# Kernel tuning notes

Hardware: AMD Instinct MI355X
Metric: run time of the kernel (lower is better)

## Reference

```python
import jax, jax.numpy as jnp
import numpy as np

D_MODEL = 128
NUM_LAYERS = 2
D_FF = 512
VOCAB = 128
OUT_DIM = 10
B, S = 512, 256
EPS_FEAT = 1e-6
LN_EPS = 1e-5


def _pos_encoding(seq_len, d):
    pos = jnp.arange(seq_len, dtype=jnp.float32)[:, None]            # [S,1]
    div = jnp.exp(jnp.arange(0, d, 2, dtype=jnp.float32) * (-np.log(10000.0) / d))
    ang = pos * div                                                   # [S,D/2]
    pe = jnp.stack([jnp.sin(ang), jnp.cos(ang)], axis=-1).reshape(seq_len, d)
    return pe[:, None, :]                                             # [S,1,D]


def _layer_norm(x, g, b):
    mu = jnp.mean(x, axis=-1, keepdims=True)
    var = jnp.mean(jnp.square(x - mu), axis=-1, keepdims=True)
    return (x - mu) * jax.lax.rsqrt(var + LN_EPS) * g + b


def setup_inputs() -> dict:
    key = jax.random.key(0)
    ks = jax.random.split(key, 20)
    sc = 0.02
    inp = {
        'src': jax.random.randint(ks[0], (B, S), 0, VOCAB),
        'emb': jax.random.normal(ks[1], (VOCAB, D_MODEL), jnp.float32) * sc,
        'wq': jax.random.normal(ks[2], (NUM_LAYERS, D_MODEL, D_MODEL), jnp.float32) * sc,
        'bq': jnp.zeros((NUM_LAYERS, D_MODEL), jnp.float32),
        'wk': jax.random.normal(ks[3], (NUM_LAYERS, D_MODEL, D_MODEL), jnp.float32) * sc,
        'bk': jnp.zeros((NUM_LAYERS, D_MODEL), jnp.float32),
        'wv': jax.random.normal(ks[4], (NUM_LAYERS, D_MODEL, D_MODEL), jnp.float32) * sc,
        'bv': jnp.zeros((NUM_LAYERS, D_MODEL), jnp.float32),
        'w1': jax.random.normal(ks[5], (NUM_LAYERS, D_FF, D_MODEL), jnp.float32) * sc,
        'b1': jnp.zeros((NUM_LAYERS, D_FF), jnp.float32),
        'w2': jax.random.normal(ks[6], (NUM_LAYERS, D_MODEL, D_FF), jnp.float32) * sc,
        'b2': jnp.zeros((NUM_LAYERS, D_MODEL), jnp.float32),
        'g1': jnp.ones((NUM_LAYERS, D_MODEL), jnp.float32),
        'beta1': jnp.zeros((NUM_LAYERS, D_MODEL), jnp.float32),
        'g2': jnp.ones((NUM_LAYERS, D_MODEL), jnp.float32),
        'beta2': jnp.zeros((NUM_LAYERS, D_MODEL), jnp.float32),
        'fc_w': jax.random.normal(ks[7], (OUT_DIM, D_MODEL), jnp.float32) * sc,
        'fc_b': jnp.zeros((OUT_DIM,), jnp.float32),
    }
    return inp


def reference(src, emb, wq, bq, wk, bk, wv, bv, w1, b1, w2, b2,
              g1, beta1, g2, beta2, fc_w, fc_b):
    # src: [B,S] int -> permute -> [S,B]
    x = emb[src.T] * np.sqrt(float(D_MODEL))          # [S,B,D]
    x = x + _pos_encoding(x.shape[0], D_MODEL)
    for l in range(NUM_LAYERS):
        # Linear attention (faithful to original: einsum 'b' axis = seq here)
        Q = jax.nn.relu(jnp.einsum('sbd,ed->sbe', x, wq[l]) + bq[l]) + EPS_FEAT
        K = jax.nn.relu(jnp.einsum('sbd,ed->sbe', x, wk[l]) + bk[l]) + EPS_FEAT
        V = jnp.einsum('sbd,ed->sbe', x, wv[l]) + bv[l]
        KV = jnp.einsum('snd,sne->sde', K, V)         # [S,D,D] (n = batch axis)
        Z = 1.0 / (jnp.einsum('snd,sd->sn', Q, K.sum(axis=1)) + EPS_FEAT)  # [S,B]
        attn = jnp.einsum('snd,sde,sn->sne', Q, KV, Z)  # [S,B,D]
        x = _layer_norm(x + attn, g1[l], beta1[l])
        ff = jnp.einsum('sbf,df->sbd',
                        jax.nn.relu(jnp.einsum('sbd,fd->sbf', x, w1[l]) + b1[l]),
                        w2[l]) + b2[l]
        x = _layer_norm(x + ff, g2[l], beta2[l])
    x = jnp.transpose(x, (1, 0, 2))                   # [B,S,D]
    pooled = jnp.mean(x, axis=1)                      # [B,D]
    return pooled @ fc_w.T + fc_b                     # [B,OUT]
```

## Files before the change

### kernel.cpp

```cpp
#include <hip/hip_runtime.h>

typedef unsigned short u16;
typedef unsigned int u32;
typedef short bf16x8 __attribute__((ext_vector_type(8)));
typedef float f32x4 __attribute__((ext_vector_type(4)));

__device__ __forceinline__ float b2f(u16 v) { return __uint_as_float(((u32)v) << 16); }
__device__ __forceinline__ u16 f2b(float f) {
    u32 x = __float_as_uint(f);
    return (u16)((x + 0x7fffu + ((x >> 16) & 1u)) >> 16);
}
__device__ __forceinline__ float lo16(u32 w) { return __uint_as_float(w << 16); }
__device__ __forceinline__ float hi16(u32 w) { return __uint_as_float(w & 0xffff0000u); }

#define S_LEN 256
#define B_SZ  512
#define DM    128
#define DFF   512
#define MROWS (S_LEN * B_SZ)

__device__ __forceinline__ int sw16(int r, int d) {
    return r * 128 + ((((d >> 3) ^ (r & 15)) & 15) << 3) + (d & 7);
}

__global__ __launch_bounds__(256) void detect_kernel(const u32* __restrict__ embw,
                                                     int* __restrict__ flag) {
    int z = 0, big = 0;
    for (int i = threadIdx.x; i < 8192; i += 256) {
        u32 w = embw[i];
        u32 lo = w & 0xffffu;
        if (lo == 0u) z++;
        else if (((lo >> 7) & 0xffu) >= 0xC0u) big++;
    }
#pragma unroll
    for (int off = 32; off > 0; off >>= 1) {
        z   += __shfl_xor(z, off, 64);
        big += __shfl_xor(big, off, 64);
    }
    __shared__ int zz[4], bb[4];
    if ((threadIdx.x & 63) == 0) { zz[threadIdx.x >> 6] = z; bb[threadIdx.x >> 6] = big; }
    __syncthreads();
    if (threadIdx.x == 0) {
        int Z = zz[0] + zz[1] + zz[2] + zz[3];
        int Bc = bb[0] + bb[1] + bb[2] + bb[3];
        flag[0] = (Z > 4096 || Bc > 16) ? 1 : 0;
    }
}

struct Ptrs { const void* p[17]; };

__global__ __launch_bounds__(256) void convert_kernel(Ptrs ps, u16* __restrict__ canon,
                                                      const int* __restrict__ flag) {
    const int cnt[17] = {16384,32768,256,32768,256,32768,256,131072,1024,131072,
                         256,256,256,256,256,1280,10};
    const int off[17] = {0,16384,49152,49408,82176,82432,115200,115456,246528,
                         247552,378624,378880,379136,379392,379648,379904,381184};
    const int bst[18] = {0,8,24,25,41,42,58,59,123,124,188,189,190,191,192,193,194,195};
    const int isf = *flag;
    const int blk = blockIdx.x;
    int idx = 0;
#pragma unroll
    for (int i = 0; i < 17; ++i) if (blk >= bst[i + 1]) idx = i + 1;
    const int local = blk - bst[idx];
    const int n = cnt[idx];
    const void* sp = ps.p[idx];
    u16* dp = canon + off[idx];
#pragma unroll
    for (int j = 0; j < 8; ++j) {
        int e = local * 2048 + j * 256 + threadIdx.x;
        if (e < n) {
            u16 v = isf ? f2b(((const float*)sp)[e]) : ((const u16*)sp)[e];
            dp[e] = v;
        }
    }
}

__global__ __launch_bounds__(256) void embed_kernel(const int* __restrict__ src,
                                                    const u16* __restrict__ emb,
                                                    u16* __restrict__ X) {
    int idx = blockIdx.x * 256 + threadIdx.x;
    int d2 = idx & 63;
    int m = idx >> 6;
    int s = m >> 9;
    int b = m & 511;
    int tok = src[b * S_LEN + s];
    int d = d2 * 2;
    float e0 = b2f(emb[tok * DM + d])     * 11.3137084989847604f;
    float e1 = b2f(emb[tok * DM + d + 1]) * 11.3137084989847604f;
    float ang = (float)s * expf((float)d * -0.0719557841560639f);
    float v0 = e0 + sinf(ang);
    float v1 = e1 + cosf(ang);
    u32 w = (u32)f2b(v0) | ((u32)f2b(v1) << 16);
    *(u32*)(X + (size_t)m * DM + d) = w;
}

__global__ __launch_bounds__(256) void kvproj_kernel(
    const u16* __restrict__ X, const u16* __restrict__ Wk, const u16* __restrict__ bk,
    const u16* __restrict__ Wv, const u16* __restrict__ bv,
    u16* __restrict__ KVt, float* __restrict__ Ksum)
{
    __shared__ __align__(16) char sm_[49152];
    u16* Xs = (u16*)sm_;
    u16* Kt = (u16*)(sm_ + 16384);
    u16* Vt = (u16*)(sm_ + 32768);
    const int s = blockIdx.x, t = threadIdx.x;
    const int w = t >> 6, quad = (t >> 4) & 3, lr = t & 15;
    const u16* Xg = X + (size_t)s * B_SZ * DM;

    bf16x8 wkf[2][4], wvf[2][4];
    float kb[2], vb[2];
#pragma unroll
    for (int ct = 0; ct < 2; ++ct) {
        int e = w * 32 + ct * 16 + lr;
#pragma unroll
        for (int kc = 0; kc < 4; ++kc) {
            wkf[ct][kc] = *(const bf16x8*)(Wk + e * 128 + kc * 32 + quad * 8);
            wvf[ct][kc] = *(const bf16x8*)(Wv + e * 128 + kc * 32 + quad * 8);
        }
        kb[ct] = b2f(bk[e]);
        vb[ct] = b2f(bv[e]);
    }

    const f32x4 z4 = {0.f, 0.f, 0.f, 0.f};
    f32x4 kvacc[2][8];
#pragma unroll
    for (int dt = 0; dt < 2; ++dt)
#pragma unroll
        for (int ct = 0; ct < 8; ++ct) kvacc[dt][ct] = z4;
    float ks[2] = {0.f, 0.f};

    for (int b0 = 0; b0 < B_SZ; b0 += 64) {
        __syncthreads();
#pragma unroll
        for (int i = 0; i < 4; ++i) {
            int e8 = (i * 256 + t) * 8; int r = e8 >> 7, k0 = e8 & 127;
            *(uint4*)(Xs + sw16(r, k0)) = *(const uint4*)(Xg + (size_t)(b0 + r) * DM + k0);
        }
        __syncthreads();
        f32x4 pa[4][2];
#pragma unroll
        for (int mt = 0; mt < 4; ++mt) { pa[mt][0] = z4; pa[mt][1] = z4; }
#pragma unroll
        for (int kc = 0; kc < 4; ++kc) {
            bf16x8 a[4];
#pragma unroll
            for (int mt = 0; mt < 4; ++mt)
                a[mt] = *(const bf16x8*)(Xs + sw16(mt * 16 + lr, kc * 32 + quad * 8));
#pragma unroll
            for (int ct = 0; ct < 2; ++ct)
#pragma unroll
                for (int mt = 0; mt < 4; ++mt)
                    pa[mt][ct] = __builtin_amdgcn_mfma_f32_16x16x32_bf16(a[mt], wkf[ct][kc], pa[mt][ct], 0, 0, 0);
        }
#pragma unroll
        for (int ct = 0; ct < 2; ++ct) {
            int e = w * 32 + ct * 16 + lr, e7 = e & 7;
#pragma unroll
            for (int mt = 0; mt < 4; ++mt) {
                u16 h[4]; float ssum = 0.f;
#pragma unroll
                for (int j = 0; j < 4; ++j) {
                    float v = fmaxf(pa[mt][ct][j] + kb[ct], 0.f) + 1e-6f;
                    h[j] = f2b(v); ssum += b2f(h[j]);
                }
                ks[ct] += ssum;
                uint2 pk; pk.x = (u32)h[0] | ((u32)h[1] << 16); pk.y = (u32)h[2] | ((u32)h[3] << 16);
                int bs = mt * 2 + (quad >> 1);
                *(uint2*)(Kt + e * 64 + (((bs ^ e7) & 7) << 3) + (quad & 1) * 4) = pk;
            }
        }
#pragma unroll
        for (int mt = 0; mt < 4; ++mt) { pa[mt][0] = z4; pa[mt][1] = z4; }
#pragma unroll
        for (int kc = 0; kc < 4; ++kc) {
            bf16x8 a[4];
#pragma unroll
            for (int mt = 0; mt < 4; ++mt)
                a[mt] = *(const bf16x8*)(Xs + sw16(mt * 16 + lr, kc * 32 + quad * 8));
#pragma unroll
            for (int ct = 0; ct < 2; ++ct)
#pragma unroll
                for (int mt = 0; mt < 4; ++mt)
                    pa[mt][ct] = __builtin_amdgcn_mfma_f32_16x16x32_bf16(a[mt], wvf[ct][kc], pa[mt][ct], 0, 0, 0);
        }
#pragma unroll
        for (int ct = 0; ct < 2; ++ct) {
            int e = w * 32 + ct * 16 + lr, e7 = e & 7;
#pragma unroll
            for (int mt = 0; mt < 4; ++mt) {
                u16 h[4];
#pragma unroll
                for (int j = 0; j < 4; ++j) h[j] = f2b(pa[mt][ct][j] + vb[ct]);
                uint2 pk; pk.x = (u32)h[0] | ((u32)h[1] << 16); pk.y = (u32)h[2] | ((u32)h[3] << 16);
                int bs = mt * 2 + (quad >> 1);
                *(uint2*)(Vt + e * 64 + (((bs ^ e7) & 7) << 3) + (quad & 1) * 4) = pk;
            }
        }
        __syncthreads();
#pragma unroll
        for (int kc = 0; kc < 2; ++kc) {
            bf16x8 ka[2];
#pragma unroll
            for (int dt = 0; dt < 2; ++dt) {
                int d = (2 * w + dt) * 16 + lr;
                ka[dt] = *(const bf16x8*)(Kt + d * 64 + ((((kc * 4 + quad) ^ (d & 7)) & 7) << 3));
            }
#pragma unroll
            for (int ct = 0; ct < 8; ++ct) {
                int e = ct * 16 + lr;
                bf16x8 vf = *(const bf16x8*)(Vt + e * 64 + ((((kc * 4 + quad) ^ (e & 7)) & 7) << 3));
                kvacc[0][ct] = __builtin_amdgcn_mfma_f32_16x16x32_bf16(ka[0], vf, kvacc[0][ct], 0, 0, 0);
                kvacc[1][ct] = __builtin_amdgcn_mfma_f32_16x16x32_bf16(ka[1], vf, kvacc[1][ct], 0, 0, 0);
            }
        }
    }
#pragma unroll
    for (int ct = 0; ct < 2; ++ct) {
        float v = ks[ct];
        v += __shfl_xor(v, 16, 64);
        v += __shfl_xor(v, 32, 64);
        if (quad == 0) Ksum[s * 128 + w * 32 + ct * 16 + lr] = v;
    }
    u16* KVg = KVt + (size_t)s * (DM * DM);
#pragma unroll
    for (int dt = 0; dt < 2; ++dt) {
        int d0 = (2 * w + dt) * 16 + quad * 4;
#pragma unroll
        for (int ct = 0; ct < 8; ++ct) {
            int e = ct * 16 + lr;
            u16 h[4];
#pragma unroll
            for (int j = 0; j < 4; ++j) h[j] = f2b(kvacc[dt][ct][j]);
            uint2 pk; pk.x = (u32)h[0] | ((u32)h[1] << 16); pk.y = (u32)h[2] | ((u32)h[3] << 16);
            *(uint2*)(KVg + e * 128 + d0) = pk;
        }
    }
}

__global__ __launch_bounds__(256) void attn_ln_kernel(
    const u16* X, const u16* __restrict__ Wq, const u16* __restrict__ bq,
    const u16* __restrict__ KVt, const float* __restrict__ Ksum,
    u16* Xout, const u16* __restrict__ g, const u16* __restrict__ beta)
{
    __shared__ __align__(16) char sm_[65536];
    u16* R1 = (u16*)sm_;
    u16* R2 = (u16*)(sm_ + 32768);
    const int blk = blockIdx.x, s = blk >> 2, rc = blk & 3, t = threadIdx.x;
    const int w = t >> 6, quad = (t >> 4) & 3, lr = t & 15;
    const size_t m0 = (size_t)s * B_SZ + rc * 128;

#pragma unroll
    for (int i = 0; i < 8; ++i) {
        int e8 = (i * 256 + t) * 8; int r = e8 >> 7, k0 = e8 & 127;
        *(uint4*)(R1 + sw16(r, k0)) = *(const uint4*)(Wq + e8);
        *(uint4*)(R2 + sw16(r, k0)) = *(const uint4*)(X + (m0 + r) * DM + k0);
    }
    __syncthreads();
    const f32x4 z4 = {0.f, 0.f, 0.f, 0.f};
    f32x4 qacc[2][8];
#pragma unroll
    for (int mt = 0; mt < 2; ++mt)
#pragma unroll
        for (int ct = 0; ct < 8; ++ct) qacc[mt][ct] = z4;
#pragma unroll
    for (int kc = 0; kc < 4; ++kc) {
        bf16x8 a[2];
#pragma unroll
        for (int mt = 0; mt < 2; ++mt)
            a[mt] = *(const bf16x8*)(R2 + sw16(w * 32 + mt * 16 + lr, kc * 32 + quad * 8));
#pragma unroll
        for (int ct = 0; ct < 8; ++ct) {
            bf16x8 wf = *(const bf16x8*)(R1 + sw16(ct * 16 + lr, kc * 32 + quad * 8));
            qacc[0][ct] = __builtin_amdgcn_mfma_f32_16x16x32_bf16(a[0], wf, qacc[0][ct], 0, 0, 0);
            qacc[1][ct] = __builtin_amdgcn_mfma_f32_16x16x32_bf16(a[1], wf, qacc[1][ct], 0, 0, 0);
        }
    }
    __syncthreads();
    float ksm[8], bqv[8];
#pragma unroll
    for (int ct = 0; ct < 8; ++ct) {
        ksm[ct] = Ksum[s * 128 + ct * 16 + lr];
        bqv[ct] = b2f(bq[ct * 16 + lr]);
    }
    float zden[2][4];
#pragma unroll
    for (int mt = 0; mt < 2; ++mt)
#pragma unroll
        for (int j = 0; j < 4; ++j) zden[mt][j] = 0.f;
#pragma unroll
    for (int mt = 0; mt < 2; ++mt)
#pragma unroll
        for (int ct = 0; ct < 8; ++ct) {
            int d = ct * 16 + lr;
#pragma unroll
            for (int j = 0; j < 4; ++j) {
                float qv = fmaxf(qacc[mt][ct][j] + bqv[ct], 0.f) + 1e-6f;
                u16 qb16 = f2b(qv);
                zden[mt][j] += b2f(qb16) * ksm[ct];
                int b = w * 32 + mt * 16 + quad * 4 + j;
                R1[sw16(b, d)] = qb16;
            }
        }
#pragma unroll
    for (int mt = 0; mt < 2; ++mt)
#pragma unroll
        for (int j = 0; j < 4; ++j) {
            float v = zden[mt][j];
            v += __shfl_xor(v, 1, 64); v += __shfl_xor(v, 2, 64);
            v += __shfl_xor(v, 4, 64); v += __shfl_xor(v, 8, 64);
            zden[mt][j] = 1.f / (v + 1e-6f);
        }
    const u16* KVg = KVt + (size_t)s * (DM * DM);
#pragma unroll
    for (int i = 0; i < 8; ++i) {
        int e8 = (i * 256 + t) * 8; int r = e8 >> 7, k0 = e8 & 127;
        *(uint4*)(R2 + sw16(r, k0)) = *(const uint4*)(KVg + e8);
    }
    __syncthreads();
    f32x4 oacc[2][8];
#pragma unroll
    for (int mt = 0; mt < 2; ++mt)
#pragma unroll
        for (int ct = 0; ct < 8; ++ct) oacc[mt][ct] = z4;
#pragma unroll
    for (int kc = 0; kc < 4; ++kc) {
        bf16x8 qa[2];
#pragma unroll
        for (int mt = 0; mt < 2; ++mt)
            qa[mt] = *(const bf16x8*)(R1 + sw16(w * 32 + mt * 16 + lr, kc * 32 + quad * 8));
#pragma unroll
        for (int ct = 0; ct < 8; ++ct) {
            bf16x8 kf = *(const bf16x8*)(R2 + sw16(ct * 16 + lr, kc * 32 + quad * 8));
            oacc[0][ct] = __builtin_amdgcn_mfma_f32_16x16x32_bf16(qa[0], kf, oacc[0][ct], 0, 0, 0);
            oacc[1][ct] = __builtin_amdgcn_mfma_f32_16x16x32_bf16(qa[1], kf, oacc[1][ct], 0, 0, 0);
        }
    }
    float gv[8], bev[8];
#pragma unroll
    for (int ct = 0; ct < 8; ++ct) {
        gv[ct]  = b2f(g[ct * 16 + lr]);
        bev[ct] = b2f(beta[ct * 16 + lr]);
    }
#pragma unroll
    for (int mt = 0; mt < 2; ++mt)
#pragma unroll
        for (int j = 0; j < 4; ++j) {
            int b = w * 32 + mt * 16 + quad * 4 + j;
            const u16* xr = X + (m0 + b) * DM;
            float vals[8], sum = 0.f, sq = 0.f;
#pragma unroll
            for (int ct = 0; ct < 8; ++ct) {
                float v = fmaf(oacc[mt][ct][j], zden[mt][j], b2f(xr[ct * 16 + lr]));
                vals[ct] = v; sum += v; sq += v * v;
            }
            sum += __shfl_xor(sum, 1, 64); sq += __shfl_xor(sq, 1, 64);
            sum += __shfl_xor(sum, 2, 64); sq += __shfl_xor(sq, 2, 64);
            sum += __shfl_xor(sum, 4, 64); sq += __shfl_xor(sq, 4, 64);
            sum += __shfl_xor(sum, 8, 64); sq += __shfl_xor(sq, 8, 64);
            float mean = sum * 0.0078125f;
            float var  = sq * 0.0078125f - mean * mean;
            float rstd = rsqrtf(fmaxf(var, 0.f) + 1e-5f);
            u16* xo = Xout + (m0 + b) * DM;
#pragma unroll
            for (int ct = 0; ct < 8; ++ct)
                xo[ct * 16 + lr] = f2b((vals[ct] - mean) * rstd * gv[ct] + bev[ct]);
        }
}

__global__ __launch_bounds__(256) void mlp_kernel(
    const u16* X, const u16* __restrict__ W1, const u16* __restrict__ b1,
    const u16* __restrict__ W2, const u16* __restrict__ b2,
    u16* Xout, const u16* __restrict__ g, const u16* __restrict__ beta)
{
    __shared__ __align__(16) char sm_[65536];
    u16* As  = (u16*)sm_;
    u16* W1c = (u16*)(sm_ + 32768);
    u16* Hc  = W1c;
    u16* W2c = (u16*)(sm_ + 49152);
    float* zs = (float*)sm_;
    const int t = threadIdx.x;
    const int m0 = blockIdx.x * 128;
    const int w  = t >> 6;
    const int lq = (t >> 4) & 3;
    const int lr = t & 15;

#pragma unroll
    for (int i = 0; i < 8; ++i) {
        int e = (i * 256 + t) * 8; int r = e >> 7, k0 = e & 127;
        *(uint4*)(As + sw16(r, k0)) = *(const uint4*)(X + (size_t)(m0 + r) * DM + k0);
    }

    const f32x4 zero4 = {0.f, 0.f, 0.f, 0.f};
    f32x4 zacc[2][8];
#pragma unroll
    for (int mt = 0; mt < 2; ++mt)
#pragma unroll
        for (int ct = 0; ct < 8; ++ct) zacc[mt][ct] = zero4;

    for (int fc = 0; fc < DFF; fc += 64) {
        __syncthreads();
#pragma unroll
        for (int i = 0; i < 4; ++i) {
            int e = (i * 256 + t) * 8; int c = e >> 7, k0 = e & 127;
            *(uint4*)(W1c + sw16(c, k0)) = *(const uint4*)(W1 + (size_t)(fc + c) * DM + k0);
        }
#pragma unroll
        for (int i = 0; i < 4; ++i) {
            int e = (i * 256 + t) * 8; int d = e >> 6, f0 = e & 63, sl = f0 >> 3;
            *(uint4*)(W2c + d * 64 + (((sl ^ (d & 7)) & 7) << 3)) =
                *(const uint4*)(W2 + (size_t)d * DFF + fc + f0);
        }
        __syncthreads();
        f32x4 hacc[2][4];
#pragma unroll
        for (int mt = 0; mt < 2; ++mt)
#pragma unroll
            for (int ct = 0; ct < 4; ++ct) hacc[mt][ct] = zero4;
#pragma unroll
        for (int kc = 0; kc < 4; ++kc) {
            bf16x8 af[2];
#pragma unroll
            for (int mt = 0; mt < 2; ++mt)
                af[mt] = *(const bf16x8*)(As + sw16(w * 32 + mt * 16 + lr, kc * 32 + lq * 8));
#pragma unroll
            for (int ct = 0; ct < 4; ++ct) {
                bf16x8 bf_ = *(const bf16x8*)(W1c + sw16(ct * 16 + lr, kc * 32 + lq * 8));
                hacc[0][ct] = __builtin_amdgcn_mfma_f32_16x16x32_bf16(af[0], bf_, hacc[0][ct], 0, 0, 0);
                hacc[1][ct] = __builtin_amdgcn_mfma_f32_16x16x32_bf16(af[1], bf_, hacc[1][ct], 0, 0, 0);
            }
        }
        __syncthreads();
#pragma unroll
        for (int ct = 0; ct < 4; ++ct) {
            int f = ct * 16 + lr;
            float hbv = b2f(b1[fc + f]);
#pragma unroll
            for (int mt = 0; mt < 2; ++mt)
#pragma unroll
                for (int j = 0; j < 4; ++j) {
                    int m = w * 32 + mt * 16 + lq * 4 + j;
                    float v = fmaxf(hacc[mt][ct][j] + hbv, 0.f);
                    Hc[m * 64 + ((((f >> 3) ^ (m & 7)) & 7) << 3) + (f & 7)] = f2b(v);
                }
        }
        __syncthreads();
#pragma unroll
        for (int kc = 0; kc < 2; ++kc) {
            bf16x8 ha[2];
#pragma unroll
            for (int mt = 0; mt < 2; ++mt) {
                int m = w * 32 + mt * 16 + lr;
                ha[mt] = *(const bf16x8*)(Hc + m * 64 + ((((kc * 4 + lq) ^ (lr & 7)) & 7) << 3));
            }
#pragma unroll
            for (int ct = 0; ct < 8; ++ct) {
                int d = ct * 16 + lr;
                bf16x8 wb = *(const bf16x8*)(W2c + d * 64 + ((((kc * 4 + lq) ^ (lr & 7)) & 7) << 3));
                zacc[0][ct] = __builtin_amdgcn_mfma_f32_16x16x32_bf16(ha[0], wb, zacc[0][ct], 0, 0, 0);
                zacc[1][ct] = __builtin_amdgcn_mfma_f32_16x16x32_bf16(ha[1], wb, zacc[1][ct], 0, 0, 0);
            }
        }
    }
    __syncthreads();
#pragma unroll
    for (int ct = 0; ct < 8; ++ct) {
        float bbv = b2f(b2[ct * 16 + lr]);
#pragma unroll
        for (int mt = 0; mt < 2; ++mt)
#pragma unroll
            for (int j = 0; j < 4; ++j) {
                int r = w * 32 + mt * 16 + lq * 4 + j;
                zs[r * 128 + ct * 16 + lr] = zacc[mt][ct][j] + bbv;
            }
    }
    __syncthreads();
    int wv = t >> 6, ln = t & 63;
    float g0 = b2f(g[ln]), g1v = b2f(g[64 + ln]);
    float be0 = b2f(beta[ln]), be1 = b2f(beta[64 + ln]);
    for (int q = 0; q < 32; ++q) {
        int r = wv * 32 + q;
        float v0 = zs[r * 128 + ln]      + b2f(X[(size_t)(m0 + r) * DM + ln]);
        float v1 = zs[r * 128 + 64 + ln] + b2f(X[(size_t)(m0 + r) * DM + 64 + ln]);
        float sum = v0 + v1, sq = v0 * v0 + v1 * v1;
#pragma unroll
        for (int off = 32; off > 0; off >>= 1) {
            sum += __shfl_xor(sum, off, 64);
            sq  += __shfl_xor(sq,  off, 64);
        }
        float mean = sum * 0.0078125f;
        float var  = sq * 0.0078125f - mean * mean;
        float rstd = rsqrtf(fmaxf(var, 0.f) + 1e-5f);
        Xout[(size_t)(m0 + r) * DM + ln]      = f2b((v0 - mean) * rstd * g0  + be0);
        Xout[(size_t)(m0 + r) * DM + 64 + ln] = f2b((v1 - mean) * rstd * g1v + be1);
    }
}

__global__ __launch_bounds__(128) void pool_fc_kernel(
    const u16* __restrict__ X, const u16* __restrict__ fcw,
    const u16* __restrict__ fcb, void* __restrict__ Out,
    const int* __restrict__ flag)
{
    __shared__ float pool[128];
    const int b = blockIdx.x, t = threadIdx.x;
    float acc = 0.f;
    for (int s = 0; s < S_LEN; ++s)
        acc += b2f(X[((size_t)s * B_SZ + b) * DM + t]);
    pool[t] = acc * (1.0f / 256.0f);
    __syncthreads();
    if (t < 10) {
        float o = b2f(fcb[t]);
        for (int d = 0; d < 128; ++d) o += pool[d] * b2f(fcw[t * 128 + d]);
        if (*flag) ((float*)Out)[b * 10 + t] = o;
        else       ((u16*)Out)[b * 10 + t] = f2b(o);
    }
}

extern "C" void kernel_launch(void* const* d_in, const int* in_sizes, int n_in,
                              void* d_out, int out_size, void* d_ws, size_t ws_size,
                              hipStream_t stream)
{
    const int* src = (const int*)d_in[0];

    char* ws = (char*)d_ws;
    u16*   X    = (u16*)ws;
    u16*   KVt  = (u16*)(ws + 33554432);
    float* Ksum = (float*)(ws + 41943040);
    int*   flag = (int*)(ws + 42074112);
    u16*   cn   = (u16*)(ws + 42074368);

    u16* emb = cn + 0;
    u16* wq  = cn + 16384;
    u16* bq  = cn + 49152;
    u16* wk  = cn + 49408;
    u16* bk  = cn + 82176;
    u16* wv  = cn + 82432;
    u16* bvp = cn + 115200;
    u16* w1  = cn + 115456;
    u16* b1  = cn + 246528;
    u16* w2  = cn + 247552;
    u16* b2  = cn + 378624;
    u16* g1  = cn + 378880;
    u16* be1 = cn + 379136;
    u16* g2  = cn + 379392;
    u16* be2 = cn + 379648;
    u16* fcw = cn + 379904;
    u16* fcb = cn + 381184;

    detect_kernel<<<1, 256, 0, stream>>>((const u32*)d_in[1], flag);

    Ptrs ps;
    for (int i = 0; i < 17; ++i) ps.p[i] = d_in[i + 1];
    convert_kernel<<<195, 256, 0, stream>>>(ps, cn, flag);

    embed_kernel<<<MROWS * 64 / 256, 256, 0, stream>>>(src, emb, X);

    for (int l = 0; l < 2; ++l) {
        kvproj_kernel<<<S_LEN, 256, 0, stream>>>(
            X, wk + l * DM * DM, bk + l * DM, wv + l * DM * DM, bvp + l * DM, KVt, Ksum);
        attn_ln_kernel<<<S_LEN * 4, 256, 0, stream>>>(
            X, wq + l * DM * DM, bq + l * DM, KVt, Ksum, X, g1 + l * DM, be1 + l * DM);
        mlp_kernel<<<MROWS / 128, 256, 0, stream>>>(
            X, w1 + l * DFF * DM, b1 + l * DFF, w2 + l * DM * DFF, b2 + l * DM,
            X, g2 + l * DM, be2 + l * DM);
    }

    pool_fc_kernel<<<B_SZ, 128, 0, stream>>>(X, fcw, fcb, d_out, flag);
}
```

Measured before the change: 446.0 us.

## Shrink MLP tile to 64 rows, keep activations in registers, fuse LN epilogue

The MLP kernel now processes 64 rows per block instead of 128. It loads the A operand straight into registers instead of staging it in shared memory, and it cuts LDS from 64KB to 40KB with a launch bound of 4 blocks per CU. The hidden tile is per-wave, so two block-wide barriers are dropped, and the residual+LayerNorm epilogue runs directly from accumulator registers with shuffles instead of a shared-memory round trip. In exchange, W1/W2 chunks are reloaded twice as often per row, and there is less MFMA reuse per weight fragment.

```diff
diff --git a/kernel.cpp b/kernel.cpp
--- a/kernel.cpp
+++ b/kernel.cpp
@@ -367,35 +367,33 @@
         }
 }
 
-__global__ __launch_bounds__(256) void mlp_kernel(
+__global__ __launch_bounds__(256, 4) void mlp_kernel(
     const u16* X, const u16* __restrict__ W1, const u16* __restrict__ b1,
     const u16* __restrict__ W2, const u16* __restrict__ b2,
     u16* Xout, const u16* __restrict__ g, const u16* __restrict__ beta)
 {
-    __shared__ __align__(16) char sm_[65536];
-    u16* As  = (u16*)sm_;
-    u16* W1c = (u16*)(sm_ + 32768);
-    u16* Hc  = W1c;
-    u16* W2c = (u16*)(sm_ + 49152);
-    float* zs = (float*)sm_;
+    __shared__ __align__(16) char sm_[40960];
+    u16* W1c = (u16*)sm_;
+    u16* W2c = (u16*)(sm_ + 16384);
+    u16* Hc  = (u16*)(sm_ + 32768);
     const int t = threadIdx.x;
-    const int m0 = blockIdx.x * 128;
+    const int m0 = blockIdx.x * 64;
     const int w  = t >> 6;
-    const int lq = (t >> 4) & 3;
+    const int quad = (t >> 4) & 3;
     const int lr = t & 15;
 
-#pragma unroll
-    for (int i = 0; i < 8; ++i) {
-        int e = (i * 256 + t) * 8; int r = e >> 7, k0 = e & 127;
-        *(uint4*)(As + sw16(r, k0)) = *(const uint4*)(X + (size_t)(m0 + r) * DM + k0);
+    bf16x8 af[4];
+    {
+        const u16* xr = X + (size_t)(m0 + w * 16 + lr) * DM + quad * 8;
+#pragma unroll
+        for (int kc = 0; kc < 4; ++kc)
+            af[kc] = *(const bf16x8*)(xr + kc * 32);
     }
 
     const f32x4 zero4 = {0.f, 0.f, 0.f, 0.f};
-    f32x4 zacc[2][8];
-#pragma unroll
-    for (int mt = 0; mt < 2; ++mt)
-#pragma unroll
-        for (int ct = 0; ct < 8; ++ct) zacc[mt][ct] = zero4;
+    f32x4 zacc[8];
+#pragma unroll
+    for (int ct = 0; ct < 8; ++ct) zacc[ct] = zero4;
 
     for (int fc = 0; fc < DFF; fc += 64) {
         __syncthreads();
@@ -411,87 +409,67 @@
                 *(const uint4*)(W2 + (size_t)d * DFF + fc + f0);
         }
         __syncthreads();
-        f32x4 hacc[2][4];
-#pragma unroll
-        for (int mt = 0; mt < 2; ++mt)
-#pragma unroll
-            for (int ct = 0; ct < 4; ++ct) hacc[mt][ct] = zero4;
-#pragma unroll
-        for (int kc = 0; kc < 4; ++kc) {
-            bf16x8 af[2];
-#pragma unroll
-            for (int mt = 0; mt < 2; ++mt)
-                af[mt] = *(const bf16x8*)(As + sw16(w * 32 + mt * 16 + lr, kc * 32 + lq * 8));
+        f32x4 hacc[4];
+#pragma unroll
+        for (int ct = 0; ct < 4; ++ct) hacc[ct] = zero4;
+#pragma unroll
+        for (int kc = 0; kc < 4; ++kc)
 #pragma unroll
             for (int ct = 0; ct < 4; ++ct) {
-                bf16x8 bf_ = *(const bf16x8*)(W1c + sw16(ct * 16 + lr, kc * 32 + lq * 8));
-                hacc[0][ct] = __builtin_amdgcn_mfma_f32_16x16x32_bf16(af[0], bf_, hacc[0][ct], 0, 0, 0);
-                hacc[1][ct] = __builtin_amdgcn_mfma_f32_16x16x32_bf16(af[1], bf_, hacc[1][ct], 0, 0, 0);
-            }
-        }
-        __syncthreads();
+                bf16x8 bf_ = *(const bf16x8*)(W1c + sw16(ct * 16 + lr, kc * 32 + quad * 8));
+                hacc[ct] = __builtin_amdgcn_mfma_f32_16x16x32_bf16(af[kc], bf_, hacc[ct], 0, 0, 0);
+            }
 #pragma unroll
         for (int ct = 0; ct < 4; ++ct) {
             int f = ct * 16 + lr;
             float hbv = b2f(b1[fc + f]);
 #pragma unroll
-            for (int mt = 0; mt < 2; ++mt)
-#pragma unroll
-                for (int j = 0; j < 4; ++j) {
-                    int m = w * 32 + mt * 16 + lq * 4 + j;
-                    float v = fmaxf(hacc[mt][ct][j] + hbv, 0.f);
-                    Hc[m * 64 + ((((f >> 3) ^ (m & 7)) & 7) << 3) + (f & 7)] = f2b(v);
-                }
-        }
-        __syncthreads();
+            for (int j = 0; j < 4; ++j) {
+                int m = w * 16 + quad * 4 + j;
+                float v = fmaxf(hacc[ct][j] + hbv, 0.f);
+                Hc[m * 64 + ((((f >> 3) ^ (m & 7)) & 7) << 3) + (f & 7)] = f2b(v);
+            }
+        }
 #pragma unroll
         for (int kc = 0; kc < 2; ++kc) {
-            bf16x8 ha[2];
-#pragma unroll
-            for (int mt = 0; mt < 2; ++mt) {
-                int m = w * 32 + mt * 16 + lr;
-                ha[mt] = *(const bf16x8*)(Hc + m * 64 + ((((kc * 4 + lq) ^ (lr & 7)) & 7) << 3));
-            }
+            int m = w * 16 + lr;
+            bf16x8 ha = *(const bf16x8*)(Hc + m * 64 + ((((kc * 4 + quad) ^ (m & 7)) & 7) << 3));
 #pragma unroll
             for (int ct = 0; ct < 8; ++ct) {
                 int d = ct * 16 + lr;
-                bf16x8 wb = *(const bf16x8*)(W2c + d * 64 + ((((kc * 4 + lq) ^ (lr & 7)) & 7) << 3));
-                zacc[0][ct] = __builtin_amdgcn_mfma_f32_16x16x32_bf16(ha[0], wb, zacc[0][ct], 0, 0, 0);
-                zacc[1][ct] = __builtin_amdgcn_mfma_f32_16x16x32_bf16(ha[1], wb, zacc[1][ct], 0, 0, 0);
-            }
-        }
-    }
-    __syncthreads();
+                bf16x8 wb = *(const bf16x8*)(W2c + d * 64 + ((((kc * 4 + quad) ^ (d & 7)) & 7) << 3));
+                zacc[ct] = __builtin_amdgcn_mfma_f32_16x16x32_bf16(ha, wb, zacc[ct], 0, 0, 0);
+            }
+        }
+    }
+    float gv[8], bev[8], bbv[8];
 #pragma unroll
     for (int ct = 0; ct < 8; ++ct) {
-        float bbv = b2f(b2[ct * 16 + lr]);
-#pragma unroll
-        for (int mt = 0; mt < 2; ++mt)
-#pragma unroll
-            for (int j = 0; j < 4; ++j) {
-                int r = w * 32 + mt * 16 + lq * 4 + j;
-                zs[r * 128 + ct * 16 + lr] = zacc[mt][ct][j] + bbv;
-            }
-    }
-    __syncthreads();
-    int wv = t >> 6, ln = t & 63;
-    float g0 = b2f(g[ln]), g1v = b2f(g[64 + ln]);
-    float be0 = b2f(beta[ln]), be1 = b2f(beta[64 + ln]);
-    for (int q = 0; q < 32; ++q) {
-        int r = wv * 32 + q;
-        float v0 = zs[r * 128 + ln]      + b2f(X[(size_t)(m0 + r) * DM + ln]);
-        float v1 = zs[r * 128 + 64 + ln] + b2f(X[(size_t)(m0 + r) * DM + 64 + ln]);
-        float sum = v0 + v1, sq = v0 * v0 + v1 * v1;
-#pragma unroll
-        for (int off = 32; off > 0; off >>= 1) {
-            sum += __shfl_xor(sum, off, 64);
-            sq  += __shfl_xor(sq,  off, 64);
-        }
+        gv[ct]  = b2f(g[ct * 16 + lr]);
+        bev[ct] = b2f(beta[ct * 16 + lr]);
+        bbv[ct] = b2f(b2[ct * 16 + lr]);
+    }
+#pragma unroll
+    for (int j = 0; j < 4; ++j) {
+        int m = w * 16 + quad * 4 + j;
+        const u16* xr = X + (size_t)(m0 + m) * DM;
+        float vals[8], sum = 0.f, sq = 0.f;
+#pragma unroll
+        for (int ct = 0; ct < 8; ++ct) {
+            float v = zacc[ct][j] + bbv[ct] + b2f(xr[ct * 16 + lr]);
+            vals[ct] = v; sum += v; sq += v * v;
+        }
+        sum += __shfl_xor(sum, 1, 64); sq += __shfl_xor(sq, 1, 64);
+        sum += __shfl_xor(sum, 2, 64); sq += __shfl_xor(sq, 2, 64);
+        sum += __shfl_xor(sum, 4, 64); sq += __shfl_xor(sq, 4, 64);
+        sum += __shfl_xor(sum, 8, 64); sq += __shfl_xor(sq, 8, 64);
         float mean = sum * 0.0078125f;
         float var  = sq * 0.0078125f - mean * mean;
         float rstd = rsqrtf(fmaxf(var, 0.f) + 1e-5f);
-        Xout[(size_t)(m0 + r) * DM + ln]      = f2b((v0 - mean) * rstd * g0  + be0);
-        Xout[(size_t)(m0 + r) * DM + 64 + ln] = f2b((v1 - mean) * rstd * g1v + be1);
+        u16* xo = Xout + (size_t)(m0 + m) * DM;
+#pragma unroll
+        for (int ct = 0; ct < 8; ++ct)
+            xo[ct * 16 + lr] = f2b((vals[ct] - mean) * rstd * gv[ct] + bev[ct]);
     }
 }
 
@@ -559,7 +537,7 @@
             X, wk + l * DM * DM, bk + l * DM, wv + l * DM * DM, bvp + l * DM, KVt, Ksum);
         attn_ln_kernel<<<S_LEN * 4, 256, 0, stream>>>(
             X, wq + l * DM * DM, bq + l * DM, KVt, Ksum, X, g1 + l * DM, be1 + l * DM);
-        mlp_kernel<<<MROWS / 128, 256, 0, stream>>>(
+        mlp_kernel<<<MROWS / 64, 256, 0, stream>>>(
             X, w1 + l * DFF * DM, b1 + l * DFF, w2 + l * DM * DFF, b2 + l * DM,
             X, g2 + l * DM, be2 + l * DM);
     }
```

Measured after the change: 434.0 us. 2.7% less time.
